# Kernel tuning notes

Measured on AMD Instinct MI355X. Metric: run time of the kernel, lower is better.

The kernel has to match this reference:

```python
import jax, jax.numpy as jnp
import numpy as np

B, P, K = 8, 8192, 16          # batches, points per batch, knn neighbors
CHANNELS = [4, 32, 64]          # input_channels + NUM_FILTERS
EPS = 1e-5                      # BatchNorm1d eps


def setup_inputs() -> dict:
    key = jax.random.key(0)
    ks = jax.random.split(key, 16)
    N = B * P
    pillar_features = jax.random.normal(ks[0], (N, CHANNELS[0]), jnp.float32)
    pos = jax.random.uniform(ks[1], (N, 3), jnp.float32) * 50.0
    batch_idx = jnp.repeat(jnp.arange(B, dtype=jnp.float32), P)
    voxel_coords = jnp.concatenate([batch_idx[:, None], pos], axis=1)  # [N,4]
    inp = {"pillar_features": pillar_features, "voxel_coords": voxel_coords}
    j = 2
    for i in range(len(CHANNELS) - 1):
        cin, cout = CHANNELS[i], CHANNELS[i + 1]
        inp[f"W{i}"] = jax.random.normal(ks[j], (cout, 2 * cin), jnp.float32) / np.sqrt(2 * cin); j += 1
        inp[f"b{i}"] = jnp.zeros((cout,), jnp.float32)
        inp[f"gamma{i}"] = jnp.ones((cout,), jnp.float32)
        inp[f"beta{i}"] = jnp.zeros((cout,), jnp.float32)
        inp[f"wk{i}"] = jax.random.normal(ks[j], (cout,), jnp.float32) / np.sqrt(cout); j += 1
        inp[f"wq{i}"] = jax.random.normal(ks[j], (cout,), jnp.float32) / np.sqrt(cout); j += 1
    return inp


def _knn(pos):
    # pos: [N,3]; equal-sized batches of P points (batch_idx = repeat(arange(B), P))
    pb = pos.reshape(B, P, 3)
    def per_batch(p):  # p: [P,3]
        d = jnp.sum((p[:, None, :] - p[None, :, :]) ** 2, axis=-1)  # [P,P]
        _, idx = jax.lax.top_k(-d, K)                               # k nearest (incl. self)
        return idx
    idx = jax.lax.map(per_batch, pb)                                # [B,P,K], one PxP at a time
    return (idx + (jnp.arange(B) * P)[:, None, None]).reshape(B * P, K)


def _edgeconv(x, idx, pos, W, b, gamma, beta, wk, wq):
    # x: [N,F], idx: [N,K] int, pos: [N,3]
    xi = x[:, None, :]                                  # [N,1,F]
    xj = x[idx]                                         # [N,K,F] gather
    e = jnp.concatenate([jnp.broadcast_to(xi, xj.shape), xj - xi], axis=-1)  # [N,K,2F]
    h = jnp.einsum('nke,oe->nok', e, W) + b[None, :, None]  # 1x1 Conv1d -> [N,O,K]
    h = jax.nn.relu(h)
    # BatchNorm1d (training-mode stats over N and K per channel, biased var)
    mu = jnp.mean(h, axis=(0, 2), keepdims=True)
    var = jnp.mean(jnp.square(h - mu), axis=(0, 2), keepdims=True)
    h = (h - mu) * jax.lax.rsqrt(var + EPS) * gamma[None, :, None] + beta[None, :, None]
    # attention: K^T Q -> [N,K,K], softmax over dim 1, feature @ att
    Kv = jnp.einsum('nok,o->nk', h, wk)
    Qv = jnp.einsum('nok,o->nk', h, wq)
    att = jax.nn.softmax(Kv[:, :, None] * Qv[:, None, :], axis=1)  # [N,K,K]
    h = jnp.einsum('nok,nkq->noq', h, att)
    # distance-based sigmoid scaling then max over neighbors
    vec = pos[idx] - pos[:, None, :]                    # [N,K,3]
    dis = jnp.sqrt(jnp.sum(vec * vec, axis=-1))         # [N,K]
    scale = 2.0 * jax.nn.sigmoid(-dis)                  # [N,K]
    return jnp.max(scale[:, None, :] * h, axis=-1)      # [N,O]


def reference(pillar_features, voxel_coords,
              W0, b0, gamma0, beta0, wk0, wq0,
              W1, b1, gamma1, beta1, wk1, wq1):
    pos = voxel_coords[:, 1:4]
    idx = _knn(jax.lax.stop_gradient(pos))  # torch knn is under no_grad
    x = pillar_features                      # [N,4]
    x = _edgeconv(x, idx, pos, W0, b0, gamma0, beta0, wk0, wq0)
    x = _edgeconv(x, idx, pos, W1, b1, gamma1, beta1, wk1, wq1)
    return (x, voxel_coords)
```

## Files before the change

kernel.cpp:

```cpp
#include <hip/hip_runtime.h>
#include <hip/hip_fp16.h>
#include <math.h>

#define B_ 8
#define P_ 8192
#define N_ 65536
#define K_ 16
#define EPS_ 1e-5f
#define NBK 1024
#define BSCALE 20.48f

__global__ __launch_bounds__(256) void init_bins(int* counts, int* cursors,
                                                 int* xminI, int* xmaxI) {
    int i = blockIdx.x * 256 + threadIdx.x;
    counts[i] = 0; cursors[i] = 0;
    xminI[i] = 0x7F7FFFFF;
    xmaxI[i] = 0x80000000;
}

__device__ __forceinline__ int bucket_of(float x) {
    int b = (int)(x * BSCALE);
    return b > (NBK - 1) ? (NBK - 1) : (b < 0 ? 0 : b);
}

__global__ __launch_bounds__(256) void count_kernel(const float* __restrict__ vc,
                                                    int* counts, int* xminI, int* xmaxI) {
    int q = blockIdx.x * 256 + threadIdx.x;
    float4 p = ((const float4*)vc)[q];
    int b = q >> 13;
    int bk = bucket_of(p.y);
    int e = b * NBK + bk;
    atomicAdd(&counts[e], 1);
    int xb = __float_as_int(p.y);
    atomicMin(&xminI[e], xb);
    atomicMax(&xmaxI[e], xb);
}

__global__ __launch_bounds__(1024) void scan_kernel(const int* __restrict__ counts,
                                                    const int* __restrict__ xminI,
                                                    const int* __restrict__ xmaxI,
                                                    int* off, float* xlub, float* xglb) {
    __shared__ int   smi[NBK];
    __shared__ float smf[NBK];
    int b = blockIdx.x, t = threadIdx.x;
    int e = b * NBK + t;

    int c = counts[e];
    smi[t] = c; __syncthreads();
    for (int s = 1; s < NBK; s <<= 1) {
        int u = smi[t]; int v = (t >= s) ? smi[t - s] : 0;
        __syncthreads(); smi[t] = u + v; __syncthreads();
    }
    off[b * (NBK + 1) + t] = smi[t] - c;
    if (t == NBK - 1) off[b * (NBK + 1) + NBK] = smi[t];

    float mx = c ? __int_as_float(xmaxI[e]) : -1e30f;
    smf[t] = mx; __syncthreads();
    for (int s = 1; s < NBK; s <<= 1) {
        float u = smf[t]; float v = (t >= s) ? smf[t - s] : -1e30f;
        __syncthreads(); smf[t] = fmaxf(u, v); __syncthreads();
    }
    xlub[e] = smf[t];
    __syncthreads();

    int r = NBK - 1 - t;
    int cr_ = counts[b * NBK + r];
    float mn = cr_ ? __int_as_float(xminI[b * NBK + r]) : 1e30f;
    smf[t] = mn; __syncthreads();
    for (int s = 1; s < NBK; s <<= 1) {
        float u = smf[t]; float v = (t >= s) ? smf[t - s] : 1e30f;
        __syncthreads(); smf[t] = fminf(u, v); __syncthreads();
    }
    xglb[b * NBK + r] = smf[t];
}

__global__ __launch_bounds__(256) void scatter_kernel(const float* __restrict__ vc,
                                                      const int* __restrict__ off,
                                                      int* cursors, float4* pos4s) {
    int q = blockIdx.x * 256 + threadIdx.x;
    float4 p = ((const float4*)vc)[q];
    int b = q >> 13;
    int bk = bucket_of(p.y);
    int slot = off[b * (NBK + 1) + bk] + atomicAdd(&cursors[b * NBK + bk], 1);
    pos4s[(b << 13) + slot] = make_float4(p.y, p.z, p.w, __int_as_float(q));
}

__global__ __launch_bounds__(256, 4) void knn3_kernel(const float4* __restrict__ pos4s,
                                                   const float* __restrict__ xlub,
                                                   const float* __restrict__ xglb,
                                                   unsigned short* __restrict__ idx_out,
                                                   __half* __restrict__ scal_out) {
    const int tid   = threadIdx.x;
    const int sub   = tid & 3;
    const int bb    = blockIdx.x >> 7;
    const int bbase = bb << 13;
    const int wq    = blockIdx.x & 127;
    const int home0 = bbase + ((wq >> 2) << 8);
    const int qslot = bbase + (wq << 6) + (tid >> 2);
    const float4 me = pos4s[qslot];
    const float qx = me.x, qy = me.y, qz = me.z;
    const int q = __float_as_int(me.w);
    const float* xl = xlub + (bb << 10);
    const float* xg = xglb + (bb << 10);

    __shared__ __align__(16) float4 tile[256];
    __shared__ int sflags[2];

    const double KINF = __longlong_as_double(0x7F800000LL << 16);
    double bd[16];
#pragma unroll
    for (int t = 0; t < 16; ++t) bd[t] = KINF;
    float bd15f = __builtin_huge_valf();
    float sbdf  = __builtin_huge_valf();

    auto CLEAN16 = [](double* m) {
#pragma unroll
        for (int dd = 8; dd >= 1; dd >>= 1)
#pragma unroll
            for (int i = 0; i < 16; ++i)
                if ((i & dd) == 0) {
                    double lo = fmin(m[i], m[i | dd]);
                    m[i | dd] = fmax(m[i], m[i | dd]);
                    m[i] = lo;
                }
    };

    auto QUAD16K = [&]() -> double {
        double m[16];
#pragma unroll
        for (int i = 0; i < 16; ++i)
            m[i] = fmin(bd[i], __shfl_xor(bd[15 - i], 1, 64));
        CLEAN16(m);
        double t = 0.0;
#pragma unroll
        for (int i = 0; i < 16; ++i)
            t = fmax(t, fmin(m[i], __shfl_xor(m[15 - i], 2, 64)));
        return t;
    };

#define DIST_(c)                                                            \
    float dx = __fsub_rn(qx, (c).x);                                        \
    float dy = __fsub_rn(qy, (c).y);                                        \
    float dz = __fsub_rn(qz, (c).z);                                        \
    float d  = __fadd_rn(__fadd_rn(__fmul_rn(dx,dx), __fmul_rn(dy,dy)),     \
                         __fmul_rn(dz,dz));

#define SCAN_(base, cntT) {                                                 \
    __syncthreads();                                                        \
    if (tid < (cntT)) tile[tid] = pos4s[(base) + tid];                      \
    __syncthreads();                                                        \
    float g_ = fminf(bd15f, sbdf);                                          \
    _Pragma("unroll 4")                                                     \
    for (int j = sub; j < (cntT); j += 4) {                                 \
        float4 c = tile[j];                                                 \
        DIST_(c)                                                            \
        if (d <= g_) {                                                      \
            double key = __longlong_as_double(                              \
                ((long long)((unsigned long long)__float_as_uint(d) << 16)) \
                | (long long)(unsigned long long)((unsigned)__float_as_int(c.w) & 0xFFFFu)); \
            _Pragma("unroll")                                               \
            for (int t = 15; t > 0; --t)                                    \
                bd[t] = fmin(bd[t], fmax(bd[t-1], key));                    \
            bd[0] = fmin(bd[0], key);                                       \
            bd15f = __uint_as_float((unsigned)                              \
                ((unsigned long long)__double_as_longlong(bd[15]) >> 16));  \
            g_ = fminf(bd15f, sbdf);                                        \
        }                                                                   \
    } }

    SCAN_(home0, 256)
    int sL = home0, sR = home0 + 256;
    for (;;) {
        double sk = QUAD16K();
        sbdf = __uint_as_float((unsigned)
            ((unsigned long long)__double_as_longlong(sk) >> 16));
        bool needL = false, needR = false;
        if (sL > bbase) {
            float xb = xl[bucket_of(pos4s[sL - 1].x)];
            float t = __fsub_rn(qx, xb);
            needL = __fmul_rn(t, t) <= sbdf;
        }
        if (sR < bbase + P_) {
            float xb = xg[bucket_of(pos4s[sR].x)];
            float t = __fsub_rn(xb, qx);
            needR = __fmul_rn(t, t) <= sbdf;
        }
        if (tid == 0) { sflags[0] = 0; sflags[1] = 0; }
        __syncthreads();
        if (needL) sflags[0] = 1;
        if (needR) sflags[1] = 1;
        __syncthreads();
        int aL = sflags[0], aR = sflags[1];
        if (!aL && !aR) break;
        if (aL) { int c_ = min(256, sL - bbase);       SCAN_(sL - c_, c_) sL -= c_; }
        if (aR) { int c_ = min(256, bbase + P_ - sR);  SCAN_(sR, c_)      sR += c_; }
    }

    double m[16];
#pragma unroll
    for (int i = 0; i < 16; ++i)
        m[i] = fmin(bd[i], __shfl_xor(bd[15 - i], 1, 64));
    CLEAN16(m);
    double u[16];
#pragma unroll
    for (int i = 0; i < 16; ++i)
        u[i] = fmin(m[i], __shfl_xor(m[15 - i], 2, 64));
    CLEAN16(u);

    if (sub == 0) {
        unsigned long long kk[16];
#pragma unroll
        for (int t = 0; t < 16; ++t)
            kk[t] = (unsigned long long)__double_as_longlong(u[t]);

        ushort4* i4 = (ushort4*)(idx_out + (size_t)q * K_);
        i4[0] = make_ushort4((unsigned short)(kk[0] & 0xFFFFu), (unsigned short)(kk[1] & 0xFFFFu),
                             (unsigned short)(kk[2] & 0xFFFFu), (unsigned short)(kk[3] & 0xFFFFu));
        i4[1] = make_ushort4((unsigned short)(kk[4] & 0xFFFFu), (unsigned short)(kk[5] & 0xFFFFu),
                             (unsigned short)(kk[6] & 0xFFFFu), (unsigned short)(kk[7] & 0xFFFFu));
        i4[2] = make_ushort4((unsigned short)(kk[8] & 0xFFFFu), (unsigned short)(kk[9] & 0xFFFFu),
                             (unsigned short)(kk[10] & 0xFFFFu), (unsigned short)(kk[11] & 0xFFFFu));
        i4[3] = make_ushort4((unsigned short)(kk[12] & 0xFFFFu), (unsigned short)(kk[13] & 0xFFFFu),
                             (unsigned short)(kk[14] & 0xFFFFu), (unsigned short)(kk[15] & 0xFFFFu));

        unsigned pw[8];
#pragma unroll
        for (int i = 0; i < 8; ++i) {
            float d0 = __uint_as_float((unsigned)(kk[2*i]     >> 16));
            float d1 = __uint_as_float((unsigned)(kk[2*i + 1] >> 16));
            float e0 = __expf(-sqrtf(d0));
            float e1 = __expf(-sqrtf(d1));
            float s0 = 2.0f * e0 / (1.0f + e0);
            float s1 = 2.0f * e1 / (1.0f + e1);
            pw[i] = (unsigned)__half_as_ushort(__float2half_rn(s0))
                  | ((unsigned)__half_as_ushort(__float2half_rn(s1)) << 16);
        }
        uint4* s4 = (uint4*)(scal_out + (size_t)q * K_);
        s4[0] = make_uint4(pw[0], pw[1], pw[2], pw[3]);
        s4[1] = make_uint4(pw[4], pw[5], pw[6], pw[7]);
    }
#undef SCAN_
#undef DIST_
}

__global__ __launch_bounds__(256) void zgemm_all(const float* __restrict__ x1,
                                                 const float* __restrict__ W,
                                                 __half* __restrict__ z) {
    const int o  = threadIdx.x & 63;
    const int pg = threadIdx.x >> 6;
    float Wr[32];
    const float4* w4 = (const float4*)(W + o * 64 + 32);
#pragma unroll
    for (int c = 0; c < 8; ++c) {
        float4 v = w4[c];
        Wr[4*c] = v.x; Wr[4*c+1] = v.y; Wr[4*c+2] = v.z; Wr[4*c+3] = v.w;
    }
    const int m0 = blockIdx.x * 16 + pg * 4;
#pragma unroll
    for (int i = 0; i < 4; ++i) {
        const int m = m0 + i;
        const float4* xr = (const float4*)x1 + (size_t)m * 16;
        float acc = 0.f;
#pragma unroll
        for (int c = 0; c < 8; ++c) {
            float4 v = xr[c];
            acc = fmaf(Wr[4*c  ], v.x, acc);
            acc = fmaf(Wr[4*c+1], v.y, acc);
            acc = fmaf(Wr[4*c+2], v.z, acc);
            acc = fmaf(Wr[4*c+3], v.w, acc);
        }
        z[((size_t)m << 6) + o] = __float2half_rn(acc);
    }
}

template<int CIN, int COUT, bool PHA, bool USEZ>
__global__ __launch_bounds__(256) void edge_kernel(
    const float* __restrict__ x,
    const unsigned short* __restrict__ idx,
    const __half* __restrict__ scal,
    const float* __restrict__ W,
    const float* __restrict__ bias,
    const float* __restrict__ wk,
    const float* __restrict__ wq,
    const float* __restrict__ acoef,
    const float* __restrict__ ccoef,
    double* __restrict__ gsum,
    double* __restrict__ gsumsq,
    float* __restrict__ out,
    const __half* __restrict__ zbuf,
    int xs4, int ostr, int niter)
{
    constexpr int LOGC = (COUT == 64) ? 6 : 5;
    constexpr int GPW  = 64 / COUT;
    constexpr int GPB  = 4 * GPW;
    constexpr int C4   = CIN / 4;
    constexpr int SJ   = USEZ ? 4 : ((K_ + 1) * CIN);
    constexpr int HTS  = COUT + 1;
    constexpr int HTN  = PHA ? 1 : (K_ * HTS);
    constexpr int PN   = PHA ? 1 : (K_ * K_);
    constexpr int KQN  = PHA ? 1 : (2 * K_);
    constexpr int SCN  = PHA ? 1 : K_;
    constexpr int WKQN = PHA ? 1 : (2 * COUT);

    const int tid  = threadIdx.x;
    const int wave = tid >> 6;
    const int lane = tid & 63;
    const int lo   = lane & (COUT - 1);
    const int grp  = lane >> LOGC;
    const int gidx = wave * GPW + grp;

    __shared__ __align__(16) float sj_s[GPB][SJ];
    __shared__ __align__(16) float hT_s[GPB][HTN];
    __shared__ __align__(16) float p_s[GPB][PN];
    __shared__ __align__(16) float kqv_s[GPB][KQN];
    __shared__ __align__(16) float rden_s[GPB][SCN];
    __shared__ __align__(16) float scal_s[GPB][SCN];
    __shared__ __align__(16) float wkq_s[WKQN];

    float Ad[CIN];
    float Wr[USEZ ? 1 : CIN];
#pragma unroll
    for (int c = 0; c < CIN; ++c) {
        float wl = W[lo * (2*CIN) + c];
        float wr = W[lo * (2*CIN) + CIN + c];
        Ad[c] = wl - wr;
        if constexpr (!USEZ) Wr[c] = wr;
    }
    const float b_s = bias[lo];

    float a_s = 0.f, c_s = 0.f;
    if constexpr (!PHA) {
        a_s = acoef[lo]; c_s = ccoef[lo];
        if (tid < COUT)            wkq_s[tid] = wk[tid];
        else if (tid < 2*COUT)     wkq_s[tid] = wq[tid - COUT];
        __syncthreads();
    }

    double lsum = 0.0, lsq = 0.0;
    const int g0      = blockIdx.x * GPB + gidx;
    const int gstride = gridDim.x * GPB;

    for (int it = 0; it < niter; ++it) {
        const int n = g0 + it * gstride;

        float hn[K_];
        float psum = 0.f, psq = 0.f;

        if constexpr (USEZ) {
            float uacc = b_s;
            const float4* xr = (const float4*)x + (size_t)n * xs4;
#pragma unroll
            for (int c = 0; c < C4; ++c) {
                float4 v = xr[c];
                uacc = fmaf(Ad[4*c  ], v.x, uacc);
                uacc = fmaf(Ad[4*c+1], v.y, uacc);
                uacc = fmaf(Ad[4*c+2], v.z, uacc);
                uacc = fmaf(Ad[4*c+3], v.w, uacc);
            }
            const uint4* iw = (const uint4*)(idx + (size_t)n * K_);
            const uint4 ia = iw[0], ib = iw[1];
            float zk[K_];
#define GA(k, w, s) { unsigned j = ((w) >> (s)) & 0xFFFFu;                  \
                      zk[k] = __half2float(zbuf[((size_t)j << 6) + lo]); }
            GA(0,  ia.x, 0) GA(1,  ia.x, 16) GA(2,  ia.y, 0) GA(3,  ia.y, 16)
            GA(4,  ia.z, 0) GA(5,  ia.z, 16) GA(6,  ia.w, 0) GA(7,  ia.w, 16)
            GA(8,  ib.x, 0) GA(9,  ib.x, 16) GA(10, ib.y, 0) GA(11, ib.y, 16)
            GA(12, ib.z, 0) GA(13, ib.z, 16) GA(14, ib.w, 0) GA(15, ib.w, 16)
#undef GA
#pragma unroll
            for (int k = 0; k < K_; ++k) {
                float h = fmaxf(uacc + zk[k], 0.f);
                if constexpr (PHA) { psum += h; psq = fmaf(h, h, psq); }
                else               hn[k] = fmaf(a_s, h, c_s);
            }
            if constexpr (!PHA) {
                if (lo < K_)
                    scal_s[gidx][lo] = __half2float(scal[(size_t)n * K_ + lo]);
            }
            __builtin_amdgcn_wave_barrier();
        } else {
            {
                const float4* xs  = (const float4*)x;
                float4*       sj4 = (float4*)sj_s[gidx];
                constexpr int TOT4 = (K_ + 1) * C4;
#pragma unroll
                for (int e0 = 0; e0 < TOT4; e0 += COUT) {
                    int e = e0 + lo;
                    if (e < TOT4) {
                        int r = e / C4;
                        int c = e - r * C4;
                        int row = (r < K_) ? (int)idx[n * K_ + r] : n;
                        sj4[e] = xs[row * xs4 + c];
                    }
                }
            }
            if constexpr (!PHA) {
                if (lo < K_)
                    scal_s[gidx][lo] = __half2float(scal[(size_t)n * K_ + lo]);
            }
            __builtin_amdgcn_wave_barrier();

            const float* sj = sj_s[gidx];
            float t0 = b_s;
#pragma unroll
            for (int c = 0; c < C4; ++c) {
                float4 v = ((const float4*)(sj + K_ * CIN))[c];
                t0 = fmaf(Ad[4*c  ], v.x, t0);
                t0 = fmaf(Ad[4*c+1], v.y, t0);
                t0 = fmaf(Ad[4*c+2], v.z, t0);
                t0 = fmaf(Ad[4*c+3], v.w, t0);
            }
#pragma unroll
            for (int k = 0; k < K_; ++k) {
                float acc = t0;
                const float4* xrr = (const float4*)(sj + k * CIN);
#pragma unroll
                for (int c = 0; c < C4; ++c) {
                    float4 v = xrr[c];
                    acc = fmaf(Wr[4*c  ], v.x, acc);
                    acc = fmaf(Wr[4*c+1], v.y, acc);
                    acc = fmaf(Wr[4*c+2], v.z, acc);
                    acc = fmaf(Wr[4*c+3], v.w, acc);
                }
                float h = fmaxf(acc, 0.f);
                if constexpr (PHA) { psum += h; psq = fmaf(h, h, psq); }
                else               hn[k] = fmaf(a_s, h, c_s);
            }
        }

        if constexpr (PHA) {
            lsum += (double)psum;
            lsq  += (double)psq;
        }

        if constexpr (!PHA) {
            float* hT = hT_s[gidx];
#pragma unroll
            for (int k = 0; k < K_; ++k) hT[k * HTS + lo] = hn[k];
            __builtin_amdgcn_wave_barrier();

            const int kk   = lo & 15;
            const int role = lo >> 4;
            float av = 0.f;
            const float* hrow = hT + kk * HTS;
            int obase; const float* wv;
            if constexpr (COUT == 64) { obase = (role & 1) * 32; wv = wkq_s + ((role >> 1) ? COUT : 0); }
            else                      { obase = 0;               wv = wkq_s + (role ? COUT : 0); }
#pragma unroll
            for (int j = 0; j < 32; ++j)
                av = fmaf(hrow[obase + j], wv[obase + j], av);
            if constexpr (COUT == 64) {
                float sum2 = av + __shfl_xor(av, 16, 64);
                if (lo < 16)                  kqv_s[gidx][kk] = sum2;
                else if (lo >= 32 && lo < 48) kqv_s[gidx][16 + kk] = sum2;
            } else {
                kqv_s[gidx][lo] = av;
            }
            __builtin_amdgcn_wave_barrier();

            if (lo < K_) {
                const int qq = lo;
                const float qv = kqv_s[gidx][K_ + qq];
                float mx = -__builtin_huge_valf();
#pragma unroll
                for (int k = 0; k < K_; ++k) mx = fmaxf(mx, kqv_s[gidx][k] * qv);
                float den = 0.f;
#pragma unroll
                for (int k = 0; k < K_; ++k) {
                    float e = __expf(kqv_s[gidx][k] * qv - mx);
                    den += e;
                    p_s[gidx][k * K_ + qq] = e;
                }
                rden_s[gidx][qq] = 1.0f / den;
            }
            __builtin_amdgcn_wave_barrier();

            float hq[K_];
#pragma unroll
            for (int qq = 0; qq < K_; ++qq) hq[qq] = 0.f;
#pragma unroll
            for (int k = 0; k < K_; ++k) {
                const float hnk = hn[k];
                const float4* p4 = (const float4*)(p_s[gidx] + k * K_);
#pragma unroll
                for (int j = 0; j < 4; ++j) {
                    float4 v = p4[j];
                    hq[4*j  ] = fmaf(hnk, v.x, hq[4*j  ]);
                    hq[4*j+1] = fmaf(hnk, v.y, hq[4*j+1]);
                    hq[4*j+2] = fmaf(hnk, v.z, hq[4*j+2]);
                    hq[4*j+3] = fmaf(hnk, v.w, hq[4*j+3]);
                }
            }
            float res = -__builtin_huge_valf();
#pragma unroll
            for (int j = 0; j < 4; ++j) {
                float4 sc = ((const float4*)scal_s[gidx])[j];
                float4 rd = ((const float4*)rden_s[gidx])[j];
                res = fmaxf(res, sc.x * (hq[4*j  ] * rd.x));
                res = fmaxf(res, sc.y * (hq[4*j+1] * rd.y));
                res = fmaxf(res, sc.z * (hq[4*j+2] * rd.z));
                res = fmaxf(res, sc.w * (hq[4*j+3] * rd.w));
            }
            out[(size_t)n * ostr + lo] = res;
            __builtin_amdgcn_wave_barrier();
        } else {
            __builtin_amdgcn_wave_barrier();
        }
    }

    if constexpr (PHA) {
        if constexpr (COUT == 32) {
            long long bs = __double_as_longlong(lsum);
            int l0 = __shfl_xor((int)(bs & 0xffffffffLL), 32, 64);
            int h0 = __shfl_xor((int)(bs >> 32), 32, 64);
            lsum += __longlong_as_double(((long long)h0 << 32) | (unsigned long long)(unsigned int)l0);
            bs = __double_as_longlong(lsq);
            l0 = __shfl_xor((int)(bs & 0xffffffffLL), 32, 64);
            h0 = __shfl_xor((int)(bs >> 32), 32, 64);
            lsq += __longlong_as_double(((long long)h0 << 32) | (unsigned long long)(unsigned int)l0);
        }
        __shared__ double redS[4][COUT];
        __shared__ double redQ[4][COUT];
        if (lane < COUT) { redS[wave][lane] = lsum; redQ[wave][lane] = lsq; }
        __syncthreads();
        if (tid < COUT) {
            double ss = redS[0][tid] + redS[1][tid] + redS[2][tid] + redS[3][tid];
            double qq = redQ[0][tid] + redQ[1][tid] + redQ[2][tid] + redQ[3][tid];
            atomicAdd(&gsum[tid], ss);
            atomicAdd(&gsumsq[tid], qq);
        }
    }
}

__global__ void finalize_kernel(const double* __restrict__ gsum, const double* __restrict__ gsumsq,
                                const float* __restrict__ gamma, const float* __restrict__ beta,
                                float* __restrict__ a, float* __restrict__ c, int cout)
{
    int o = threadIdx.x;
    if (o < cout) {
        const double inv = 1.0 / ((double)N_ * (double)K_);
        double mu  = gsum[o] * inv;
        double var = gsumsq[o] * inv - mu * mu;
        double rs  = 1.0 / sqrt(var + (double)EPS_);
        double av  = rs * (double)gamma[o];
        a[o] = (float)av;
        c[o] = (float)((double)beta[o] - mu * av);
    }
}

__global__ __launch_bounds__(256) void copy_vc(const float4* __restrict__ src,
                                               float4* __restrict__ dst) {
    int i = blockIdx.x * 256 + threadIdx.x;
    dst[i] = src[i];
}

extern "C" void kernel_launch(void* const* d_in, const int* in_sizes, int n_in,
                              void* d_out, int out_size, void* d_ws, size_t ws_size,
                              hipStream_t stream)
{
    const float* pillar = (const float*)d_in[0];
    const float* vc     = (const float*)d_in[1];
    const float* W0  = (const float*)d_in[2];
    const float* b0  = (const float*)d_in[3];
    const float* g0  = (const float*)d_in[4];
    const float* be0 = (const float*)d_in[5];
    const float* wk0 = (const float*)d_in[6];
    const float* wq0 = (const float*)d_in[7];
    const float* W1  = (const float*)d_in[8];
    const float* b1  = (const float*)d_in[9];
    const float* g1  = (const float*)d_in[10];
    const float* be1 = (const float*)d_in[11];
    const float* wk1 = (const float*)d_in[12];
    const float* wq1 = (const float*)d_in[13];

    char* ws = (char*)d_ws;
    unsigned short* idx = (unsigned short*)ws;
    __half* scal = (__half*)(ws + (size_t)2*1024*1024);
    __half* zh   = (__half*)(ws + (size_t)4*1024*1024);
    double* dsum = (double*)(ws + 14680064);
    double *s0 = dsum, *sq0 = dsum + 64, *s1 = dsum + 128, *sq1 = dsum + 192;
    float* coef  = (float*)(ws + 14682112);
    float *a0 = coef, *c0 = coef + 64, *a1 = coef + 128, *c1 = coef + 192;
    size_t base2 = (size_t)12*1024*1024;
    float4* pos4s = (float4*)(ws + base2);
    int* counts   = (int*)(ws + base2 + (1u<<20));
    int* cursors  = counts + B_*NBK;
    int* off      = cursors + B_*NBK;
    int* xminI    = off + B_*(NBK+1);
    int* xmaxI    = xminI + B_*NBK;
    float* xlub   = (float*)(xmaxI + B_*NBK);
    float* xglb   = xlub + B_*NBK;

    float* xout = (float*)d_out;
    float* vout = xout + (size_t)N_ * 64;

    hipMemsetAsync(dsum, 0, 2048, stream);
    init_bins<<<B_*NBK/256, 256, 0, stream>>>(counts, cursors, xminI, xmaxI);
    count_kernel<<<N_/256, 256, 0, stream>>>(vc, counts, xminI, xmaxI);
    scan_kernel<<<B_, NBK, 0, stream>>>(counts, xminI, xmaxI, off, xlub, xglb);
    scatter_kernel<<<N_/256, 256, 0, stream>>>(vc, off, cursors, pos4s);
    knn3_kernel<<<N_/64, 256, 0, stream>>>(pos4s, xlub, xglb, idx, scal);

    edge_kernel<4,32,true ,false><<<1024, 256, 0, stream>>>(pillar, idx, scal, W0, b0, wk0, wq0,
                                                            nullptr, nullptr, s0, sq0, nullptr,
                                                            nullptr, 1, 0, 8);
    finalize_kernel<<<1, 64, 0, stream>>>(s0, sq0, g0, be0, a0, c0, 32);
    edge_kernel<4,32,false,false><<<1024, 256, 0, stream>>>(pillar, idx, scal, W0, b0, wk0, wq0,
                                                            a0, c0, nullptr, nullptr, xout,
                                                            nullptr, 1, 64, 8);

    zgemm_all<<<N_/16, 256, 0, stream>>>(xout, W1, zh);
    edge_kernel<32,64,true ,true><<<2048, 256, 0, stream>>>(xout, idx, scal, W1, b1, wk1, wq1,
                                                            nullptr, nullptr, s1, sq1, nullptr,
                                                            zh, 16, 0, 8);
    finalize_kernel<<<1, 64, 0, stream>>>(s1, sq1, g1, be1, a1, c1, 64);
    edge_kernel<32,64,false,true><<<2048, 256, 0, stream>>>(xout, idx, scal, W1, b1, wk1, wq1,
                                                            a1, c1, nullptr, nullptr, xout,
                                                            zh, 16, 64, 8);

    copy_vc<<<256, 256, 0, stream>>>((const float4*)vc, (float4*)vout);
}
```

Baseline: 552.8 us.

## Split each kNN query across eight lanes with shared pruning threshold

The kNN kernel now gives each query point 8 cooperating lanes instead of 4, with 32 queries per block and twice as many blocks. The top-16 merge becomes a three-step butterfly across lanes. During the scan, lanes exchange their current 16th-best distance by shuffle every iteration so the pruning threshold is the group minimum. The aim is more parallelism per query, shorter per-lane candidate loops and tighter pruning, traded for more shuffle and merge work plus higher register-pressure targets (launch bounds 6).

New measurement: 602.9 us. 9.1% more time.

```diff
diff --git a/kernel.cpp b/kernel.cpp
--- a/kernel.cpp
+++ b/kernel.cpp
@@ -85,18 +85,18 @@
     pos4s[(b << 13) + slot] = make_float4(p.y, p.z, p.w, __int_as_float(q));
 }
 
-__global__ __launch_bounds__(256, 4) void knn3_kernel(const float4* __restrict__ pos4s,
+__global__ __launch_bounds__(256, 6) void knn3_kernel(const float4* __restrict__ pos4s,
                                                    const float* __restrict__ xlub,
                                                    const float* __restrict__ xglb,
                                                    unsigned short* __restrict__ idx_out,
                                                    __half* __restrict__ scal_out) {
     const int tid   = threadIdx.x;
-    const int sub   = tid & 3;
-    const int bb    = blockIdx.x >> 7;
+    const int sub   = tid & 7;
+    const int bb    = blockIdx.x >> 8;
     const int bbase = bb << 13;
-    const int wq    = blockIdx.x & 127;
-    const int home0 = bbase + ((wq >> 2) << 8);
-    const int qslot = bbase + (wq << 6) + (tid >> 2);
+    const int wq    = blockIdx.x & 255;
+    const int home0 = bbase + ((wq >> 3) << 8);
+    const int qslot = bbase + (wq << 5) + (tid >> 3);
     const float4 me = pos4s[qslot];
     const float qx = me.x, qy = me.y, qz = me.z;
     const int q = __float_as_int(me.w);
@@ -125,16 +125,28 @@
                 }
     };
 
-    auto QUAD16K = [&]() -> double {
+    auto MERGE16IP = [&CLEAN16](double* a, int mask) {
+#pragma unroll
+        for (int i = 0; i < 8; ++i) {
+            double lo = a[i], hi = a[15 - i];
+            double plo = __shfl_xor(lo, mask, 64);
+            double phi = __shfl_xor(hi, mask, 64);
+            a[i]      = fmin(lo, phi);
+            a[15 - i] = fmin(hi, plo);
+        }
+        CLEAN16(a);
+    };
+
+    auto OCT16K = [&]() -> double {
         double m[16];
 #pragma unroll
+        for (int i = 0; i < 16; ++i) m[i] = bd[i];
+        MERGE16IP(m, 1);
+        MERGE16IP(m, 2);
+        double t = 0.0;
+#pragma unroll
         for (int i = 0; i < 16; ++i)
-            m[i] = fmin(bd[i], __shfl_xor(bd[15 - i], 1, 64));
-        CLEAN16(m);
-        double t = 0.0;
-#pragma unroll
-        for (int i = 0; i < 16; ++i)
-            t = fmax(t, fmin(m[i], __shfl_xor(m[15 - i], 2, 64)));
+            t = fmax(t, fmin(m[i], __shfl_xor(m[15 - i], 4, 64)));
         return t;
     };
 
@@ -149,12 +161,16 @@
     __syncthreads();                                                        \
     if (tid < (cntT)) tile[tid] = pos4s[(base) + tid];                      \
     __syncthreads();                                                        \
-    float g_ = fminf(bd15f, sbdf);                                          \
     _Pragma("unroll 4")                                                     \
-    for (int j = sub; j < (cntT); j += 4) {                                 \
-        float4 c = tile[j];                                                 \
+    for (int j0 = 0; j0 < (cntT); j0 += 8) {                                \
+        float om = fminf(bd15f, __shfl_xor(bd15f, 1, 64));                  \
+        om = fminf(om, __shfl_xor(om, 2, 64));                              \
+        om = fminf(om, __shfl_xor(om, 4, 64));                              \
+        float g_ = fminf(om, sbdf);                                         \
+        int j = j0 + sub;                                                   \
+        float4 c = tile[j & 255];                                           \
         DIST_(c)                                                            \
-        if (d <= g_) {                                                      \
+        if (j < (cntT) && d <= g_) {                                        \
             double key = __longlong_as_double(                              \
                 ((long long)((unsigned long long)__float_as_uint(d) << 16)) \
                 | (long long)(unsigned long long)((unsigned)__float_as_int(c.w) & 0xFFFFu)); \
@@ -164,14 +180,13 @@
             bd[0] = fmin(bd[0], key);                                       \
             bd15f = __uint_as_float((unsigned)                              \
                 ((unsigned long long)__double_as_longlong(bd[15]) >> 16));  \
-            g_ = fminf(bd15f, sbdf);                                        \
         }                                                                   \
     } }
 
     SCAN_(home0, 256)
     int sL = home0, sR = home0 + 256;
     for (;;) {
-        double sk = QUAD16K();
+        double sk = OCT16K();
         sbdf = __uint_as_float((unsigned)
             ((unsigned long long)__double_as_longlong(sk) >> 16));
         bool needL = false, needR = false;
@@ -196,22 +211,15 @@
         if (aR) { int c_ = min(256, bbase + P_ - sR);  SCAN_(sR, c_)      sR += c_; }
     }
 
-    double m[16];
-#pragma unroll
-    for (int i = 0; i < 16; ++i)
-        m[i] = fmin(bd[i], __shfl_xor(bd[15 - i], 1, 64));
-    CLEAN16(m);
-    double u[16];
-#pragma unroll
-    for (int i = 0; i < 16; ++i)
-        u[i] = fmin(m[i], __shfl_xor(m[15 - i], 2, 64));
-    CLEAN16(u);
+    MERGE16IP(bd, 1);
+    MERGE16IP(bd, 2);
+    MERGE16IP(bd, 4);
 
     if (sub == 0) {
         unsigned long long kk[16];
 #pragma unroll
         for (int t = 0; t < 16; ++t)
-            kk[t] = (unsigned long long)__double_as_longlong(u[t]);
+            kk[t] = (unsigned long long)__double_as_longlong(bd[t]);
 
         ushort4* i4 = (ushort4*)(idx_out + (size_t)q * K_);
         i4[0] = make_ushort4((unsigned short)(kk[0] & 0xFFFFu), (unsigned short)(kk[1] & 0xFFFFu),
@@ -599,7 +607,7 @@
     count_kernel<<<N_/256, 256, 0, stream>>>(vc, counts, xminI, xmaxI);
     scan_kernel<<<B_, NBK, 0, stream>>>(counts, xminI, xmaxI, off, xlub, xglb);
     scatter_kernel<<<N_/256, 256, 0, stream>>>(vc, off, cursors, pos4s);
-    knn3_kernel<<<N_/64, 256, 0, stream>>>(pos4s, xlub, xglb, idx, scal);
+    knn3_kernel<<<N_/32, 256, 0, stream>>>(pos4s, xlub, xglb, idx, scal);
 
     edge_kernel<4,32,true ,false><<<1024, 256, 0, stream>>>(pillar, idx, scal, W0, b0, wk0, wq0,
                                                             nullptr, nullptr, s0, sq0, nullptr,
```
